# Kernel tuning notes

Measured on AMD Instinct MI355X. Metric: run time of the kernel, lower is better.

Reference implementation:

```python
import jax, jax.numpy as jnp
import numpy as np

N_EMBD = 1024
N_HEAD = 16
EPS = 1e-5

def layer_norm(x, g, b):
    mu = jnp.mean(x, axis=-1, keepdims=True)
    var = jnp.mean(jnp.square(x - mu), axis=-1, keepdims=True)
    return (x - mu) * jax.lax.rsqrt(var + EPS) * g + b

def setup_inputs() -> dict:
    key = jax.random.key(0)
    ks = jax.random.split(key, 12)
    C = N_EMBD
    s = lambda n: 1.0 / np.sqrt(n)
    return {
        "x": jax.random.normal(ks[0], (4, 2048, C), dtype=jnp.float32),
        "ln1_g": jnp.ones((C,), jnp.float32),
        "ln1_b": jnp.zeros((C,), jnp.float32),
        "attn_w": jax.random.normal(ks[1], (C, 3 * C), dtype=jnp.float32) * s(C),
        "attn_b": jnp.zeros((3 * C,), jnp.float32),
        "proj_w": jax.random.normal(ks[2], (C, C), dtype=jnp.float32) * s(C),
        "proj_b": jnp.zeros((C,), jnp.float32),
        "ln2_g": jnp.ones((C,), jnp.float32),
        "ln2_b": jnp.zeros((C,), jnp.float32),
        "fc1_w": jax.random.normal(ks[3], (C, 4 * C), dtype=jnp.float32) * s(C),
        "fc1_b": jnp.zeros((4 * C,), jnp.float32),
        "fc2_w": jax.random.normal(ks[4], (4 * C, C), dtype=jnp.float32) * s(4 * C),
        "fc2_b": jnp.zeros((C,), jnp.float32),
    }

def reference(x, ln1_g, ln1_b, attn_w, attn_b, proj_w, proj_b,
              ln2_g, ln2_b, fc1_w, fc1_b, fc2_w, fc2_b):
    B, T, C = x.shape
    H = N_HEAD
    D = C // H

    # --- self attention on ln1(x) ---
    h = layer_norm(x, ln1_g, ln1_b)
    qkv = h @ attn_w + attn_b                       # [B,T,3C]
    q, k, v = jnp.split(qkv, 3, axis=-1)
    q = q.reshape(B, T, H, D).transpose(0, 2, 1, 3)  # [B,H,T,D]
    k = k.reshape(B, T, H, D).transpose(0, 2, 1, 3)
    v = v.reshape(B, T, H, D).transpose(0, 2, 1, 3)
    att = jnp.einsum("bhqd,bhkd->bhqk", q, k) * (D ** -0.5)
    causal = jnp.tril(jnp.ones((T, T), dtype=bool))
    att = jnp.where(causal[None, None], att, -jnp.inf)
    att = jax.nn.softmax(att, axis=-1)
    y = jnp.einsum("bhqk,bhkd->bhqd", att, v)        # [B,H,T,D]
    y = y.transpose(0, 2, 1, 3).reshape(B, T, C)
    y = y @ proj_w + proj_b
    x = x + y

    # --- MLP on ln2(x) ---
    h = layer_norm(x, ln2_g, ln2_b)
    h = jax.nn.relu(h @ fc1_w + fc1_b)
    h = h @ fc2_w + fc2_b
    return x + h
```

## Files before the change

### kernel.cpp

```cpp
#include <hip/hip_runtime.h>
#include <cstdint>
#include <cstddef>

typedef __bf16 bf16x8 __attribute__((ext_vector_type(8)));
typedef float f32x4 __attribute__((ext_vector_type(4)));
typedef float f32x16 __attribute__((ext_vector_type(16)));
typedef unsigned short u16;
typedef unsigned uint2v __attribute__((ext_vector_type(2)));

namespace {
constexpr int Bb = 4, Tt = 2048, Cc = 1024, Hh = 16, Dd = 64;
constexpr int ROWS = Bb * Tt;
constexpr int C3 = 3 * Cc;
constexpr float LNEPS = 1e-5f;
constexpr float SCL2 = 0.18033688011112042f;
}

__device__ __forceinline__ u16 f2bf(float f) {
  union { float f; unsigned u; } v; v.f = f;
  return (u16)((v.u + 0x7fffu + ((v.u >> 16) & 1u)) >> 16);
}
__device__ __forceinline__ u16 bfn(float f) {
  union { __bf16 b; u16 u; } t; t.b = (__bf16)f; return t.u;
}
__device__ __forceinline__ unsigned pk2(float lo, float hi) {
  union { __bf16 b[2]; unsigned u; } t;
  t.b[0] = (__bf16)lo; t.b[1] = (__bf16)hi;
  return t.u;
}
__device__ __forceinline__ float exp2_hw(float x) {
  float r;
  asm("v_exp_f32 %0, %1" : "=v"(r) : "v"(x));
  return r;
}
__device__ __forceinline__ uint2v plswap(unsigned a, unsigned b) {
  return __builtin_amdgcn_permlane32_swap(a, b, false, false);
}
__device__ __forceinline__ float xhalf_max(float x) {
  union { float f; unsigned u; } c; c.f = x;
  uint2v r = plswap(c.u, c.u);
  union { unsigned u; float f; } a, b; a.u = r[0]; b.u = r[1];
  return fmaxf(a.f, b.f);
}
__device__ __forceinline__ float xhalf_sum(float x) {
  union { float f; unsigned u; } c; c.f = x;
  uint2v r = plswap(c.u, c.u);
  union { unsigned u; float f; } a, b; a.u = r[0]; b.u = r[1];
  return a.f + b.f;
}

typedef __attribute__((address_space(3))) unsigned lds_u32;
typedef __attribute__((address_space(1))) const unsigned glb_u32;
__device__ __forceinline__ void gload_lds16(const u16* g, u16* l) {
  __builtin_amdgcn_global_load_lds((glb_u32*)g, (lds_u32*)l, 16, 0, 0);
}

__global__ __launch_bounds__(256) void ln_kernel(
    const float* __restrict__ x, const float* __restrict__ g,
    const float* __restrict__ b, u16* __restrict__ out)
{
  const int row = blockIdx.x;
  const int tid = threadIdx.x;
  const float4 v = reinterpret_cast<const float4*>(x + (size_t)row * Cc)[tid];
  float s  = v.x + v.y + v.z + v.w;
  float ss = v.x * v.x + v.y * v.y + v.z * v.z + v.w * v.w;
#pragma unroll
  for (int off = 32; off; off >>= 1) {
    s  += __shfl_xor(s, off);
    ss += __shfl_xor(ss, off);
  }
  __shared__ float sa[4], sb[4];
  const int w = tid >> 6;
  if ((tid & 63) == 0) { sa[w] = s; sb[w] = ss; }
  __syncthreads();
  s  = sa[0] + sa[1] + sa[2] + sa[3];
  ss = sb[0] + sb[1] + sb[2] + sb[3];
  const float mu   = s * (1.0f / Cc);
  const float var  = ss * (1.0f / Cc) - mu * mu;
  const float rstd = rsqrtf(var + LNEPS);
  const float4 gv = reinterpret_cast<const float4*>(g)[tid];
  const float4 bv = reinterpret_cast<const float4*>(b)[tid];
  ushort4 o;
  o.x = f2bf((v.x - mu) * rstd * gv.x + bv.x);
  o.y = f2bf((v.y - mu) * rstd * gv.y + bv.y);
  o.z = f2bf((v.z - mu) * rstd * gv.z + bv.z);
  o.w = f2bf((v.w - mu) * rstd * gv.w + bv.w);
  reinterpret_cast<ushort4*>(out + (size_t)row * Cc)[tid] = o;
}

__global__ __launch_bounds__(256) void wcast_t(
    const float* __restrict__ w, u16* __restrict__ wt, int K, int N)
{
  __shared__ float tile[32][33];
  const int n0 = blockIdx.x * 32, k0 = blockIdx.y * 32;
  const int tx = threadIdx.x & 31, ty = threadIdx.x >> 5;
#pragma unroll
  for (int i = 0; i < 4; i++)
    tile[ty + i * 8][tx] = w[(size_t)(k0 + ty + i * 8) * N + n0 + tx];
  __syncthreads();
#pragma unroll
  for (int i = 0; i < 4; i++)
    wt[(size_t)(n0 + ty + i * 8) * K + k0 + tx] = f2bf(tile[tx][ty + i * 8]);
}

enum { EPI_BIAS_BF16 = 0, EPI_BIAS_RELU_BF16 = 1, EPI_BIAS_RES_F32 = 2 };

template <int EPI>
__global__ __launch_bounds__(512, 2) void gemm256(
    const u16* __restrict__ A, const u16* __restrict__ Bt,
    const float* __restrict__ bias, const float* __restrict__ res,
    void* __restrict__ outp, int M, int N, int K)
{
  __shared__ alignas(16) u16 Al[4][256 * 32];
  __shared__ alignas(16) u16 Bl[4][256 * 32];

  const int tid  = threadIdx.x;
  const int lane = tid & 63;
  const int wv   = tid >> 6;
  const int wr   = wv >> 2, wc = wv & 3;
  const int lr   = lane & 15;
  const int lg   = (lane >> 4) & 3;

  const int xcd = (int)blockIdx.x & 7;
  const int j   = (int)blockIdx.x >> 3;
  const int nbn = N >> 8;
  const int bmpx = ((int)gridDim.x >> 3) / nbn;
  const int bm = (xcd * bmpx + j / nbn) << 8;
  const int bn = (j % nbn) << 8;

  const int srl  = tid >> 2;
  const int schk = (tid & 3) ^ ((tid >> 3) & 3);
  const u16* gA = A  + (size_t)(bm + srl) * K + schk * 8;
  const u16* gB = Bt + (size_t)(bn + srl) * K + schk * 8;
  const size_t rowK128 = (size_t)128 * K;

  const int fsw  = (lg ^ ((lr >> 1) & 3)) * 8;
  const int arow = wr * 128 + lr;
  const int brow = wc * 64 + lr;

  f32x4 acc[8][4];
#pragma unroll
  for (int mi = 0; mi < 8; mi++)
#pragma unroll
    for (int nj = 0; nj < 4; nj++)
      acc[mi][nj] = (f32x4){0.f, 0.f, 0.f, 0.f};

  const int NT = K >> 5;

  auto stageA = [&](int t) {
    u16* d = &Al[t & 3][tid * 8];
    gload_lds16(gA + (size_t)t * 32, d);
    gload_lds16(gA + rowK128 + (size_t)t * 32, d + 4096);
  };
  auto stageB = [&](int t) {
    u16* d = &Bl[t & 3][tid * 8];
    gload_lds16(gB + (size_t)t * 32, d);
    gload_lds16(gB + rowK128 + (size_t)t * 32, d + 4096);
  };

  for (int t = 0; t < 3; ++t) { stageA(t); stageB(t); }
  asm volatile("s_waitcnt vmcnt(8)" ::: "memory");
  asm volatile("s_barrier" ::: "memory");

  for (int kt = 0; kt < NT; ++kt) {
    const u16* Ab = &Al[kt & 3][0];
    const u16* Bb = &Bl[kt & 3][0];
    const bool st = (kt + 3 < NT);

    bf16x8 bf[4];
#pragma unroll
    for (int nj = 0; nj < 4; ++nj)
      bf[nj] = *reinterpret_cast<const bf16x8*>(Bb + (brow + nj * 16) * 32 + fsw);
    bf16x8 af[4];
#pragma unroll
    for (int m = 0; m < 4; ++m)
      af[m] = *reinterpret_cast<const bf16x8*>(Ab + (arow + m * 16) * 32 + fsw);
    if (st) stageA(kt + 3);
    asm volatile("s_barrier" ::: "memory");
    __builtin_amdgcn_s_setprio(1);
#pragma unroll
    for (int m = 0; m < 4; ++m)
#pragma unroll
      for (int nj = 0; nj < 4; ++nj)
        acc[m][nj] = __builtin_amdgcn_mfma_f32_16x16x32_bf16(af[m], bf[nj], acc[m][nj], 0, 0, 0);
    __builtin_amdgcn_s_setprio(0);
    asm volatile("s_barrier" ::: "memory");

#pragma unroll
    for (int m = 0; m < 4; ++m)
      af[m] = *reinterpret_cast<const bf16x8*>(Ab + (arow + (m + 4) * 16) * 32 + fsw);
    if (st) stageB(kt + 3);
    if (kt < NT - 3)       { asm volatile("s_waitcnt vmcnt(8)" ::: "memory"); }
    else if (kt == NT - 3) { asm volatile("s_waitcnt vmcnt(4)" ::: "memory"); }
    else if (kt == NT - 2) { asm volatile("s_waitcnt vmcnt(0)" ::: "memory"); }
    asm volatile("s_barrier" ::: "memory");
    __builtin_amdgcn_s_setprio(1);
#pragma unroll
    for (int m = 0; m < 4; ++m)
#pragma unroll
      for (int nj = 0; nj < 4; ++nj)
        acc[m + 4][nj] = __builtin_amdgcn_mfma_f32_16x16x32_bf16(af[m], bf[nj], acc[m + 4][nj], 0, 0, 0);
    __builtin_amdgcn_s_setprio(0);
    asm volatile("s_barrier" ::: "memory");
  }

#pragma unroll
  for (int mi = 0; mi < 8; ++mi) {
    const int row0 = bm + wr * 128 + mi * 16 + lg * 4;
#pragma unroll
    for (int nj = 0; nj < 4; ++nj) {
      const int col = bn + wc * 64 + nj * 16 + lr;
      const float bv = bias[col];
#pragma unroll
      for (int r = 0; r < 4; ++r) {
        const int row = row0 + r;
        float v = acc[mi][nj][r] + bv;
        if constexpr (EPI == EPI_BIAS_RELU_BF16) v = fmaxf(v, 0.0f);
        if constexpr (EPI == EPI_BIAS_RES_F32) {
          float* out = (float*)outp;
          out[(size_t)row * N + col] = v + res[(size_t)row * N + col];
        } else {
          ((u16*)outp)[(size_t)row * N + col] = f2bf(v);
        }
      }
    }
  }
}

template <int EPI>
__global__ __launch_bounds__(256, 3) void gemm_bt2(
    const u16* __restrict__ A, const u16* __restrict__ Bt,
    const float* __restrict__ bias, const float* __restrict__ res,
    void* __restrict__ outp, int M, int N, int K)
{
  constexpr int BM = 128, BN = 128, BK = 64;
  __shared__ alignas(16) u16 As[BM][BK];
  __shared__ alignas(16) u16 Bs[BN][BK];
  const int tid  = threadIdx.x;
  const int lane = tid & 63;
  const int wv   = tid >> 6;
  const int wr   = wv >> 1, wc = wv & 1;
  const int lr   = lane & 15, lg = lane >> 4;

  const int xcd = (int)blockIdx.x & 7;
  const int j   = (int)blockIdx.x >> 3;
  const int bm = (xcd * 8 + (j >> 3)) << 7;
  const int bn = (j & 7) << 7;

  f32x4 acc[4][4];
#pragma unroll
  for (int mi = 0; mi < 4; mi++)
#pragma unroll
    for (int nj = 0; nj < 4; nj++)
      acc[mi][nj] = (f32x4){0.f, 0.f, 0.f, 0.f};

  const int srow = tid >> 3;
  const int scol = ((tid & 7) ^ (srow & 7)) * 8;
  const u16* ga = &A [(size_t)(bm + srow) * K + scol];
  const u16* gb = &Bt[(size_t)(bn + srow) * K + scol];
  u16* as_dst = &As[0][0] + (size_t)tid * 8;
  u16* bs_dst = &Bs[0][0] + (size_t)tid * 8;

  for (int k0 = 0; k0 < K; k0 += BK) {
#pragma unroll
    for (int p = 0; p < 4; p++) {
      gload_lds16(ga + (size_t)p * 32 * K + k0, as_dst + p * 2048);
      gload_lds16(gb + (size_t)p * 32 * K + k0, bs_dst + p * 2048);
    }
    __syncthreads();
#pragma unroll
    for (int kk = 0; kk < BK; kk += 32) {
      const int cb = kk >> 3;
      const int csw = ((cb + lg) ^ (lr & 7)) * 8;
      bf16x8 af[4], bfr[4];
#pragma unroll
      for (int mi = 0; mi < 4; mi++)
        af[mi] = *reinterpret_cast<const bf16x8*>(&As[wr * 64 + mi * 16 + lr][0] + csw);
#pragma unroll
      for (int nj = 0; nj < 4; nj++)
        bfr[nj] = *reinterpret_cast<const bf16x8*>(&Bs[wc * 64 + nj * 16 + lr][0] + csw);
#pragma unroll
      for (int mi = 0; mi < 4; mi++)
#pragma unroll
        for (int nj = 0; nj < 4; nj++)
          acc[mi][nj] = __builtin_amdgcn_mfma_f32_16x16x32_bf16(af[mi], bfr[nj], acc[mi][nj], 0, 0, 0);
    }
    __syncthreads();
  }

#pragma unroll
  for (int mi = 0; mi < 4; mi++) {
#pragma unroll
    for (int nj = 0; nj < 4; nj++) {
      const int col = bn + wc * 64 + nj * 16 + lr;
      const float bv = bias[col];
#pragma unroll
      for (int r = 0; r < 4; r++) {
        const int row = bm + wr * 64 + mi * 16 + lg * 4 + r;
        float v = acc[mi][nj][r] + bv;
        if constexpr (EPI == EPI_BIAS_RELU_BF16) v = fmaxf(v, 0.0f);
        if constexpr (EPI == EPI_BIAS_RES_F32) {
          float* out = (float*)outp;
          out[(size_t)row * N + col] = v + res[(size_t)row * N + col];
        } else {
          ((u16*)outp)[(size_t)row * N + col] = f2bf(v);
        }
      }
    }
  }
}

__global__ __launch_bounds__(256) void build_vt(
    const u16* __restrict__ qkv, u16* __restrict__ vt)
{
  __shared__ u16 tile[64][80];
  const int t0 = blockIdx.x * 64;
  const int h  = blockIdx.y;
  const int b  = blockIdx.z;
  const int tid = threadIdx.x;
  const int rr = tid >> 3, cc = (tid & 7) * 8;
#pragma unroll
  for (int p = 0; p < 2; p++) {
    const int t = rr + p * 32;
    bf16x8 v = *reinterpret_cast<const bf16x8*>(
        &qkv[(size_t)(b * Tt + t0 + t) * C3 + 2 * Cc + h * Dd + cc]);
    *reinterpret_cast<bf16x8*>(&tile[t][cc]) = v;
  }
  __syncthreads();
#pragma unroll
  for (int p = 0; p < 2; p++) {
    const int d = rr + p * 32;
    union { u16 u[8]; int4 v; } o;
#pragma unroll
    for (int j = 0; j < 8; j++) o.u[j] = tile[cc + j][d];
    *reinterpret_cast<int4*>(&vt[(size_t)((b * Hh + h) * Dd + d) * Tt + t0 + cc]) = o.v;
  }
}

__global__ __launch_bounds__(512, 2) void flash_attn(
    const u16* __restrict__ qkv,
    const u16* __restrict__ vt,
    u16* __restrict__ y)
{
  const int tid = threadIdx.x, lane = tid & 63, wv = tid >> 6;
  const int l31 = lane & 31, hf = lane >> 5;

  const int bid = blockIdx.x;
  const int lid = (bid & 7) * 32 + (bid >> 3);
  const int bh = lid >> 2, pg = lid & 3;
  const int b = bh >> 4, h = bh & 15;
  const int sbase = pg * 4 + (wv & 3);
  const int s = (wv < 4) ? sbase : (31 - sbase);

  const u16* qbase = qkv + (size_t)b * Tt * C3 + h * Dd;
  const u16* kbase = qbase + Cc;
  const u16* vbase = vt + (size_t)bh * Dd * Tt;

  bool dmask[16];
#pragma unroll
  for (int r = 0; r < 16; r++)
    dmask[r] = ((r & 3) + 8 * (r >> 2) + 4 * hf) > l31;

  const int qa0 = s * 64;
  const int qb0 = qa0 + 32;
  const int ta = 2 * s;

  bf16x8 qfa[4], qfb[4];
#pragma unroll
  for (int kc = 0; kc < 4; kc++) {
    qfa[kc] = *reinterpret_cast<const bf16x8*>(
        &qbase[(size_t)(qa0 + l31) * C3 + kc * 16 + hf * 8]);
    qfb[kc] = *reinterpret_cast<const bf16x8*>(
        &qbase[(size_t)(qb0 + l31) * C3 + kc * 16 + hf * 8]);
  }

  f32x16 oa[2], ob[2];
#pragma unroll
  for (int i = 0; i < 16; i++) { oa[0][i] = 0.f; oa[1][i] = 0.f; ob[0][i] = 0.f; ob[1][i] = 0.f; }
  float mA = -INFINITY, lA = 0.0f, mB = -INFINITY, lB = 0.0f;

  const u16* kptr = &kbase[(size_t)l31 * C3 + hf * 8];
  const u16* vp0 = &vbase[(size_t)l31 * Tt + hf * 8];
  const u16* vp1 = vp0 + (size_t)32 * Tt;

  bf16x8 kf[4];
#pragma unroll
  for (int kc = 0; kc < 4; kc++)
    kf[kc] = *reinterpret_cast<const bf16x8*>(kptr + kc * 16);

  for (int kt = 0; kt <= ta; ++kt) {
    bf16x8 vf[2][2];
#pragma unroll
    for (int ch = 0; ch < 2; ch++) {
      vf[0][ch] = *reinterpret_cast<const bf16x8*>(vp0 + ch * 16);
      vf[1][ch] = *reinterpret_cast<const bf16x8*>(vp1 + ch * 16);
    }
    vp0 += 32; vp1 += 32;

    f32x16 sA, sB;
#pragma unroll
    for (int i = 0; i < 16; i++) { sA[i] = 0.f; sB[i] = 0.f; }
#pragma unroll
    for (int kc = 0; kc < 4; kc++) {
      sA = __builtin_amdgcn_mfma_f32_32x32x16_bf16(kf[kc], qfa[kc], sA, 0, 0, 0);
      sB = __builtin_amdgcn_mfma_f32_32x32x16_bf16(kf[kc], qfb[kc], sB, 0, 0, 0);
    }

    kptr += (size_t)32 * C3;
    bf16x8 kn[4];
#pragma unroll
    for (int kc = 0; kc < 4; kc++)
      kn[kc] = *reinterpret_cast<const bf16x8*>(kptr + kc * 16);

    const bool diagA = (kt == ta);

    float svA[16], svB[16];
#pragma unroll
    for (int r = 0; r < 16; r++) {
      svA[r] = sA[r];
      if (diagA && dmask[r]) svA[r] = -INFINITY;
      svB[r] = sB[r];
    }

    float mAa = fmaxf(fmaxf(svA[0], svA[1]), fmaxf(svA[2], svA[3]));
    float mAb = fmaxf(fmaxf(svA[4], svA[5]), fmaxf(svA[6], svA[7]));
    float mAc = fmaxf(fmaxf(svA[8], svA[9]), fmaxf(svA[10], svA[11]));
    float mAd = fmaxf(fmaxf(svA[12], svA[13]), fmaxf(svA[14], svA[15]));
    float m8A = fmaxf(fmaxf(mAa, mAb), fmaxf(mAc, mAd));
    float mBa = fmaxf(fmaxf(svB[0], svB[1]), fmaxf(svB[2], svB[3]));
    float mBb = fmaxf(fmaxf(svB[4], svB[5]), fmaxf(svB[6], svB[7]));
    float mBc = fmaxf(fmaxf(svB[8], svB[9]), fmaxf(svB[10], svB[11]));
    float mBd = fmaxf(fmaxf(svB[12], svB[13]), fmaxf(svB[14], svB[15]));
    float m8B = fmaxf(fmaxf(mBa, mBb), fmaxf(mBc, mBd));
    m8A = xhalf_max(m8A);
    m8B = xhalf_max(m8B);

    if (!__all(m8A - mA <= 64.0f)) {
      const float mnew  = fmaxf(mA, m8A);
      const float alpha = exp2_hw((mA - mnew) * SCL2);
      lA *= alpha;
#pragma unroll
      for (int i = 0; i < 16; i++) { oa[0][i] *= alpha; oa[1][i] *= alpha; }
      mA = mnew;
    }
    if (!__all(m8B - mB <= 64.0f)) {
      const float mnew  = fmaxf(mB, m8B);
      const float alpha = exp2_hw((mB - mnew) * SCL2);
      lB *= alpha;
#pragma unroll
      for (int i = 0; i < 16; i++) { ob[0][i] *= alpha; ob[1][i] *= alpha; }
      mB = mnew;
    }

    const float msA = mA * SCL2;
    const float msB = mB * SCL2;
    float pA[16], pB[16];
#pragma unroll
    for (int r = 0; r < 16; r++) {
      pA[r] = exp2_hw(fmaf(svA[r], SCL2, -msA));
      pB[r] = exp2_hw(fmaf(svB[r], SCL2, -msB));
    }
    {
      float a0 = ((pA[0] + pA[1]) + (pA[2] + pA[3])) + ((pA[4] + pA[5]) + (pA[6] + pA[7]));
      float a1 = ((pA[8] + pA[9]) + (pA[10] + pA[11])) + ((pA[12] + pA[13]) + (pA[14] + pA[15]));
      lA += a0 + a1;
      float b0 = ((pB[0] + pB[1]) + (pB[2] + pB[3])) + ((pB[4] + pB[5]) + (pB[6] + pB[7]));
      float b1 = ((pB[8] + pB[9]) + (pB[10] + pB[11])) + ((pB[12] + pB[13]) + (pB[14] + pB[15]));
      lB += b0 + b1;
    }

    unsigned pwA[2][4], pwB[2][4];
#pragma unroll
    for (int ch = 0; ch < 2; ch++) {
      const int bs = ch * 8;
      {
        unsigned w0 = pk2(pA[bs + 0], pA[bs + 1]);
        unsigned w1 = pk2(pA[bs + 2], pA[bs + 3]);
        unsigned w2 = pk2(pA[bs + 4], pA[bs + 5]);
        unsigned w3 = pk2(pA[bs + 6], pA[bs + 7]);
        uint2v r02 = plswap(w0, w2);
        uint2v r13 = plswap(w1, w3);
        pwA[ch][0] = r02[0]; pwA[ch][2] = r02[1];
        pwA[ch][1] = r13[0]; pwA[ch][3] = r13[1];
      }
      {
        unsigned w0 = pk2(pB[bs + 0], pB[bs + 1]);
        unsigned w1 = pk2(pB[bs + 2], pB[bs + 3]);
        unsigned w2 = pk2(pB[bs + 4], pB[bs + 5]);
        unsigned w3 = pk2(pB[bs + 6], pB[bs + 7]);
        uint2v r02 = plswap(w0, w2);
        uint2v r13 = plswap(w1, w3);
        pwB[ch][0] = r02[0]; pwB[ch][2] = r02[1];
        pwB[ch][1] = r13[0]; pwB[ch][3] = r13[1];
      }
    }

#pragma unroll
    for (int d0i = 0; d0i < 2; d0i++)
#pragma unroll
      for (int ch = 0; ch < 2; ch++) {
        union { unsigned w[4]; bf16x8 v; } pa, pb;
        pa.w[0] = pwA[ch][0]; pa.w[1] = pwA[ch][1];
        pa.w[2] = pwA[ch][2]; pa.w[3] = pwA[ch][3];
        pb.w[0] = pwB[ch][0]; pb.w[1] = pwB[ch][1];
        pb.w[2] = pwB[ch][2]; pb.w[3] = pwB[ch][3];
        oa[d0i] = __builtin_amdgcn_mfma_f32_32x32x16_bf16(vf[d0i][ch], pa.v, oa[d0i], 0, 0, 0);
        ob[d0i] = __builtin_amdgcn_mfma_f32_32x32x16_bf16(vf[d0i][ch], pb.v, ob[d0i], 0, 0, 0);
      }

#pragma unroll
    for (int kc = 0; kc < 4; kc++) kf[kc] = kn[kc];
  }

  {
    bf16x8 vf[2][2];
#pragma unroll
    for (int ch = 0; ch < 2; ch++) {
      vf[0][ch] = *reinterpret_cast<const bf16x8*>(vp0 + ch * 16);
      vf[1][ch] = *reinterpret_cast<const bf16x8*>(vp1 + ch * 16);
    }

    f32x16 sB;
#pragma unroll
    for (int i = 0; i < 16; i++) sB[i] = 0.f;
#pragma unroll
    for (int kc = 0; kc < 4; kc++)
      sB = __builtin_amdgcn_mfma_f32_32x32x16_bf16(kf[kc], qfb[kc], sB, 0, 0, 0);

    float svB[16];
#pragma unroll
    for (int r = 0; r < 16; r++) {
      svB[r] = sB[r];
      if (dmask[r]) svB[r] = -INFINITY;
    }
    float mBa = fmaxf(fmaxf(svB[0], svB[1]), fmaxf(svB[2], svB[3]));
    float mBb = fmaxf(fmaxf(svB[4], svB[5]), fmaxf(svB[6], svB[7]));
    float mBc = fmaxf(fmaxf(svB[8], svB[9]), fmaxf(svB[10], svB[11]));
    float mBd = fmaxf(fmaxf(svB[12], svB[13]), fmaxf(svB[14], svB[15]));
    float m8B = fmaxf(fmaxf(mBa, mBb), fmaxf(mBc, mBd));
    m8B = xhalf_max(m8B);

    if (!__all(m8B - mB <= 64.0f)) {
      const float mnew  = fmaxf(mB, m8B);
      const float alpha = exp2_hw((mB - mnew) * SCL2);
      lB *= alpha;
#pragma unroll
      for (int i = 0; i < 16; i++) { ob[0][i] *= alpha; ob[1][i] *= alpha; }
      mB = mnew;
    }
    const float msB = mB * SCL2;
    float pB[16];
#pragma unroll
    for (int r = 0; r < 16; r++)
      pB[r] = exp2_hw(fmaf(svB[r], SCL2, -msB));
    {
      float b0 = ((pB[0] + pB[1]) + (pB[2] + pB[3])) + ((pB[4] + pB[5]) + (pB[6] + pB[7]));
      float b1 = ((pB[8] + pB[9]) + (pB[10] + pB[11])) + ((pB[12] + pB[13]) + (pB[14] + pB[15]));
      lB += b0 + b1;
    }
    unsigned pwB[2][4];
#pragma unroll
    for (int ch = 0; ch < 2; ch++) {
      const int bs = ch * 8;
      unsigned w0 = pk2(pB[bs + 0], pB[bs + 1]);
      unsigned w1 = pk2(pB[bs + 2], pB[bs + 3]);
      unsigned w2 = pk2(pB[bs + 4], pB[bs + 5]);
      unsigned w3 = pk2(pB[bs + 6], pB[bs + 7]);
      uint2v r02 = plswap(w0, w2);
      uint2v r13 = plswap(w1, w3);
      pwB[ch][0] = r02[0]; pwB[ch][2] = r02[1];
      pwB[ch][1] = r13[0]; pwB[ch][3] = r13[1];
    }
#pragma unroll
    for (int d0i = 0; d0i < 2; d0i++)
#pragma unroll
      for (int ch = 0; ch < 2; ch++) {
        union { unsigned w[4]; bf16x8 v; } pb;
        pb.w[0] = pwB[ch][0]; pb.w[1] = pwB[ch][1];
        pb.w[2] = pwB[ch][2]; pb.w[3] = pwB[ch][3];
        ob[d0i] = __builtin_amdgcn_mfma_f32_32x32x16_bf16(vf[d0i][ch], pb.v, ob[d0i], 0, 0, 0);
      }
  }

  {
    const float lsA = xhalf_sum(lA);
    const float invA = 1.0f / lsA;
    u16* yrow = y + (size_t)(b * Tt + qa0 + l31) * Cc + h * Dd;
#pragma unroll
    for (int d0i = 0; d0i < 2; d0i++)
#pragma unroll
      for (int qd = 0; qd < 4; qd++) {
        ushort4 o;
        o.x = bfn(oa[d0i][qd * 4 + 0] * invA);
        o.y = bfn(oa[d0i][qd * 4 + 1] * invA);
        o.z = bfn(oa[d0i][qd * 4 + 2] * invA);
        o.w = bfn(oa[d0i][qd * 4 + 3] * invA);
        *reinterpret_cast<ushort4*>(&yrow[d0i * 32 + qd * 8 + hf * 4]) = o;
      }
  }
  {
    const float lsB = xhalf_sum(lB);
    const float invB = 1.0f / lsB;
    u16* yrow = y + (size_t)(b * Tt + qb0 + l31) * Cc + h * Dd;
#pragma unroll
    for (int d0i = 0; d0i < 2; d0i++)
#pragma unroll
      for (int qd = 0; qd < 4; qd++) {
        ushort4 o;
        o.x = bfn(ob[d0i][qd * 4 + 0] * invB);
        o.y = bfn(ob[d0i][qd * 4 + 1] * invB);
        o.z = bfn(ob[d0i][qd * 4 + 2] * invB);
        o.w = bfn(ob[d0i][qd * 4 + 3] * invB);
        *reinterpret_cast<ushort4*>(&yrow[d0i * 32 + qd * 8 + hf * 4]) = o;
      }
  }
}

extern "C" void kernel_launch(void* const* d_in, const int* in_sizes, int n_in,
                              void* d_out, int out_size, void* d_ws, size_t ws_size,
                              hipStream_t stream)
{
  const float* x      = (const float*)d_in[0];
  const float* ln1_g  = (const float*)d_in[1];
  const float* ln1_b  = (const float*)d_in[2];
  const float* attn_w = (const float*)d_in[3];
  const float* attn_b = (const float*)d_in[4];
  const float* proj_w = (const float*)d_in[5];
  const float* proj_b = (const float*)d_in[6];
  const float* ln2_g  = (const float*)d_in[7];
  const float* ln2_b  = (const float*)d_in[8];
  const float* fc1_w  = (const float*)d_in[9];
  const float* fc1_b  = (const float*)d_in[10];
  const float* fc2_w  = (const float*)d_in[11];
  const float* fc2_b  = (const float*)d_in[12];
  float* out = (float*)d_out;

  char* ws = (char*)d_ws;
  size_t o = 0;
  auto alloc = [&](size_t bytes) { char* p = ws + o; o += bytes; return p; };
  u16* wqkv_t  = (u16*)alloc((size_t)C3 * Cc * 2);
  u16* wproj_t = (u16*)alloc((size_t)Cc * Cc * 2);
  u16* wfc1_t  = (u16*)alloc((size_t)4096 * Cc * 2);
  u16* wfc2_t  = (u16*)alloc((size_t)Cc * 4096 * 2);
  u16* h_bf    = (u16*)alloc((size_t)ROWS * Cc * 2);
  u16* y_bf    = (u16*)alloc((size_t)ROWS * Cc * 2);
  u16* qkv_raw = (u16*)alloc((size_t)ROWS * C3 * 2);
  u16* vt      = (u16*)alloc((size_t)Bb * Hh * Dd * Tt * 2);
  u16* hh      = qkv_raw;

  wcast_t<<<dim3(C3 / 32, Cc / 32), 256, 0, stream>>>(attn_w, wqkv_t, Cc, C3);
  wcast_t<<<dim3(Cc / 32, Cc / 32), 256, 0, stream>>>(proj_w, wproj_t, Cc, Cc);
  wcast_t<<<dim3(4096 / 32, Cc / 32), 256, 0, stream>>>(fc1_w, wfc1_t, Cc, 4096);
  wcast_t<<<dim3(Cc / 32, 4096 / 32), 256, 0, stream>>>(fc2_w, wfc2_t, 4096, Cc);

  ln_kernel<<<ROWS, 256, 0, stream>>>(x, ln1_g, ln1_b, h_bf);
  gemm256<EPI_BIAS_BF16><<<32 * (C3 / 256), 512, 0, stream>>>(
      h_bf, wqkv_t, attn_b, nullptr, qkv_raw, ROWS, C3, Cc);
  build_vt<<<dim3(Tt / 64, Hh, Bb), 256, 0, stream>>>(qkv_raw, vt);
  flash_attn<<<dim3(256), 512, 0, stream>>>(qkv_raw, vt, y_bf);
  gemm_bt2<EPI_BIAS_RES_F32><<<512, 256, 0, stream>>>(
      y_bf, wproj_t, proj_b, x, out, ROWS, Cc, Cc);
  ln_kernel<<<ROWS, 256, 0, stream>>>(out, ln2_g, ln2_b, h_bf);
  gemm256<EPI_BIAS_RELU_BF16><<<32 * (4096 / 256), 512, 0, stream>>>(
      h_bf, wfc1_t, fc1_b, nullptr, hh, ROWS, 4096, Cc);
  gemm_bt2<EPI_BIAS_RES_F32><<<512, 256, 0, stream>>>(
      hh, wfc2_t, fc2_b, out, out, ROWS, Cc, 4096);
}
```

Before: 365.2 us.

## Restructure 256x256 GEMM into 8-phase ping-pong pipeline with BK=64 half-tiles

Replaces the 4-stage BK=32 GEMM used for the QKV and FC1 projections with a double-buffered BK=64 kernel. Each 256x256 tile is split into A and B halves of 128 rows, and the work runs as four MFMA phases. The next tile's half loads are interleaved between phases using explicit vmcnt waits and barriers. Warp-to-output mapping changes so each warp covers scattered 64x32 sub-blocks, which means more LDS reads and barriers per tile in exchange for larger K chunks. The gemm_bt2 grid mapping is generalized to compute the tile count from N, which leaves the launch configuration the same.

Result: no change. 359.6 us (-1.5%).

```diff
diff --git a/kernel.cpp b/kernel.cpp
--- a/kernel.cpp
+++ b/kernel.cpp
@@ -106,20 +106,21 @@
 enum { EPI_BIAS_BF16 = 0, EPI_BIAS_RELU_BF16 = 1, EPI_BIAS_RES_F32 = 2 };
 
 template <int EPI>
-__global__ __launch_bounds__(512, 2) void gemm256(
+__global__ __launch_bounds__(512, 2) void gemm8p(
     const u16* __restrict__ A, const u16* __restrict__ Bt,
     const float* __restrict__ bias, const float* __restrict__ res,
     void* __restrict__ outp, int M, int N, int K)
 {
-  __shared__ alignas(16) u16 Al[4][256 * 32];
-  __shared__ alignas(16) u16 Bl[4][256 * 32];
-
-  const int tid  = threadIdx.x;
-  const int lane = tid & 63;
-  const int wv   = tid >> 6;
-  const int wr   = wv >> 2, wc = wv & 3;
-  const int lr   = lane & 15;
-  const int lg   = (lane >> 4) & 3;
+  __shared__ alignas(16) u16 Asl[2][2][128 * 64];
+  __shared__ alignas(16) u16 Bsl[2][2][128 * 64];
+
+  const int tid = threadIdx.x;
+  const int l   = tid & 63;
+  const int wv  = tid >> 6;
+  const int wr  = wv >> 2;
+  const int wc  = wv & 3;
+  const int lr  = l & 15;
+  const int lg  = (l >> 4) & 3;
 
   const int xcd = (int)blockIdx.x & 7;
   const int j   = (int)blockIdx.x >> 3;
@@ -128,15 +129,14 @@
   const int bm = (xcd * bmpx + j / nbn) << 8;
   const int bn = (j % nbn) << 8;
 
-  const int srl  = tid >> 2;
-  const int schk = (tid & 3) ^ ((tid >> 3) & 3);
-  const u16* gA = A  + (size_t)(bm + srl) * K + schk * 8;
-  const u16* gB = Bt + (size_t)(bn + srl) * K + schk * 8;
-  const size_t rowK128 = (size_t)128 * K;
-
-  const int fsw  = (lg ^ ((lr >> 1) & 3)) * 8;
-  const int arow = wr * 128 + lr;
-  const int brow = wc * 64 + lr;
+  const int srw = wv * 8 + (l >> 3);
+  const int sch = ((l & 7) ^ ((l >> 3) & 7)) * 8;
+  const int dst = (l & 7) * 8;
+
+  const int csw0 = (lg ^ (lr & 7)) * 8;
+  const int csw1 = ((4 + lg) ^ (lr & 7)) * 8;
+  const int ar = wr * 64;
+  const int br = wc * 32;
 
   f32x4 acc[8][4];
 #pragma unroll
@@ -145,71 +145,117 @@
     for (int nj = 0; nj < 4; nj++)
       acc[mi][nj] = (f32x4){0.f, 0.f, 0.f, 0.f};
 
-  const int NT = K >> 5;
-
-  auto stageA = [&](int t) {
-    u16* d = &Al[t & 3][tid * 8];
-    gload_lds16(gA + (size_t)t * 32, d);
-    gload_lds16(gA + rowK128 + (size_t)t * 32, d + 4096);
+  const int NT = K >> 6;
+
+  auto stA = [&](int h, int tt) {
+#pragma unroll
+    for (int L = 0; L < 2; ++L)
+      gload_lds16(A + (size_t)(bm + h * 128 + L * 64 + srw) * K + tt * 64 + sch,
+                  &Asl[tt & 1][h][(L * 64 + srw) * 64 + dst]);
   };
-  auto stageB = [&](int t) {
-    u16* d = &Bl[t & 3][tid * 8];
-    gload_lds16(gB + (size_t)t * 32, d);
-    gload_lds16(gB + rowK128 + (size_t)t * 32, d + 4096);
+  auto stB = [&](int h, int tt) {
+#pragma unroll
+    for (int L = 0; L < 2; ++L)
+      gload_lds16(Bt + (size_t)(bn + h * 128 + L * 64 + srw) * K + tt * 64 + sch,
+                  &Bsl[tt & 1][h][(L * 64 + srw) * 64 + dst]);
   };
 
-  for (int t = 0; t < 3; ++t) { stageA(t); stageB(t); }
-  asm volatile("s_waitcnt vmcnt(8)" ::: "memory");
+  stA(0, 0); stB(0, 0); stB(1, 0); stA(1, 0);
+  asm volatile("s_waitcnt vmcnt(4)" ::: "memory");
   asm volatile("s_barrier" ::: "memory");
 
-  for (int kt = 0; kt < NT; ++kt) {
-    const u16* Ab = &Al[kt & 3][0];
-    const u16* Bb = &Bl[kt & 3][0];
-    const bool st = (kt + 3 < NT);
-
-    bf16x8 bf[4];
-#pragma unroll
-    for (int nj = 0; nj < 4; ++nj)
-      bf[nj] = *reinterpret_cast<const bf16x8*>(Bb + (brow + nj * 16) * 32 + fsw);
-    bf16x8 af[4];
-#pragma unroll
-    for (int m = 0; m < 4; ++m)
-      af[m] = *reinterpret_cast<const bf16x8*>(Ab + (arow + m * 16) * 32 + fsw);
-    if (st) stageA(kt + 3);
+  bf16x8 af[4][2], bfr[2][2][2];
+
+  for (int t = 0; t < NT; ++t) {
+    const int cb = t & 1;
+    const bool st = (t + 1 < NT);
+    const u16* Ah0 = &Asl[cb][0][0];
+    const u16* Ah1 = &Asl[cb][1][0];
+    const u16* Bh0 = &Bsl[cb][0][0];
+    const u16* Bh1 = &Bsl[cb][1][0];
+
+#pragma unroll
+    for (int m = 0; m < 4; ++m) {
+      af[m][0] = *reinterpret_cast<const bf16x8*>(Ah0 + (ar + m * 16 + lr) * 64 + csw0);
+      af[m][1] = *reinterpret_cast<const bf16x8*>(Ah0 + (ar + m * 16 + lr) * 64 + csw1);
+    }
+#pragma unroll
+    for (int n = 0; n < 2; ++n) {
+      bfr[0][n][0] = *reinterpret_cast<const bf16x8*>(Bh0 + (br + n * 16 + lr) * 64 + csw0);
+      bfr[0][n][1] = *reinterpret_cast<const bf16x8*>(Bh0 + (br + n * 16 + lr) * 64 + csw1);
+    }
+    if (st) { stA(0, t + 1); stB(0, t + 1); }
     asm volatile("s_barrier" ::: "memory");
     __builtin_amdgcn_s_setprio(1);
 #pragma unroll
     for (int m = 0; m < 4; ++m)
 #pragma unroll
-      for (int nj = 0; nj < 4; ++nj)
-        acc[m][nj] = __builtin_amdgcn_mfma_f32_16x16x32_bf16(af[m], bf[nj], acc[m][nj], 0, 0, 0);
+      for (int n = 0; n < 2; ++n) {
+        acc[m][n] = __builtin_amdgcn_mfma_f32_16x16x32_bf16(af[m][0], bfr[0][n][0], acc[m][n], 0, 0, 0);
+        acc[m][n] = __builtin_amdgcn_mfma_f32_16x16x32_bf16(af[m][1], bfr[0][n][1], acc[m][n], 0, 0, 0);
+      }
+    __builtin_amdgcn_s_setprio(0);
+    if (st) asm volatile("s_waitcnt vmcnt(6)" ::: "memory");
+    else    asm volatile("s_waitcnt vmcnt(2)" ::: "memory");
+    asm volatile("s_barrier" ::: "memory");
+
+#pragma unroll
+    for (int n = 0; n < 2; ++n) {
+      bfr[1][n][0] = *reinterpret_cast<const bf16x8*>(Bh1 + (br + n * 16 + lr) * 64 + csw0);
+      bfr[1][n][1] = *reinterpret_cast<const bf16x8*>(Bh1 + (br + n * 16 + lr) * 64 + csw1);
+    }
+    if (st) stB(1, t + 1);
+    asm volatile("s_barrier" ::: "memory");
+    __builtin_amdgcn_s_setprio(1);
+#pragma unroll
+    for (int m = 0; m < 4; ++m)
+#pragma unroll
+      for (int n = 0; n < 2; ++n) {
+        acc[m][2 + n] = __builtin_amdgcn_mfma_f32_16x16x32_bf16(af[m][0], bfr[1][n][0], acc[m][2 + n], 0, 0, 0);
+        acc[m][2 + n] = __builtin_amdgcn_mfma_f32_16x16x32_bf16(af[m][1], bfr[1][n][1], acc[m][2 + n], 0, 0, 0);
+      }
+    __builtin_amdgcn_s_setprio(0);
+    if (st) asm volatile("s_waitcnt vmcnt(6)" ::: "memory");
+    else    asm volatile("s_waitcnt vmcnt(0)" ::: "memory");
+    asm volatile("s_barrier" ::: "memory");
+
+#pragma unroll
+    for (int m = 0; m < 4; ++m) {
+      af[m][0] = *reinterpret_cast<const bf16x8*>(Ah1 + (ar + m * 16 + lr) * 64 + csw0);
+      af[m][1] = *reinterpret_cast<const bf16x8*>(Ah1 + (ar + m * 16 + lr) * 64 + csw1);
+    }
+    if (st) stA(1, t + 1);
+    asm volatile("s_barrier" ::: "memory");
+    __builtin_amdgcn_s_setprio(1);
+#pragma unroll
+    for (int m = 0; m < 4; ++m)
+#pragma unroll
+      for (int n = 0; n < 2; ++n) {
+        acc[4 + m][n] = __builtin_amdgcn_mfma_f32_16x16x32_bf16(af[m][0], bfr[0][n][0], acc[4 + m][n], 0, 0, 0);
+        acc[4 + m][n] = __builtin_amdgcn_mfma_f32_16x16x32_bf16(af[m][1], bfr[0][n][1], acc[4 + m][n], 0, 0, 0);
+      }
     __builtin_amdgcn_s_setprio(0);
     asm volatile("s_barrier" ::: "memory");
 
+    __builtin_amdgcn_s_setprio(1);
 #pragma unroll
     for (int m = 0; m < 4; ++m)
-      af[m] = *reinterpret_cast<const bf16x8*>(Ab + (arow + (m + 4) * 16) * 32 + fsw);
-    if (st) stageB(kt + 3);
-    if (kt < NT - 3)       { asm volatile("s_waitcnt vmcnt(8)" ::: "memory"); }
-    else if (kt == NT - 3) { asm volatile("s_waitcnt vmcnt(4)" ::: "memory"); }
-    else if (kt == NT - 2) { asm volatile("s_waitcnt vmcnt(0)" ::: "memory"); }
+#pragma unroll
+      for (int n = 0; n < 2; ++n) {
+        acc[4 + m][2 + n] = __builtin_amdgcn_mfma_f32_16x16x32_bf16(af[m][0], bfr[1][n][0], acc[4 + m][2 + n], 0, 0, 0);
+        acc[4 + m][2 + n] = __builtin_amdgcn_mfma_f32_16x16x32_bf16(af[m][1], bfr[1][n][1], acc[4 + m][2 + n], 0, 0, 0);
+      }
+    __builtin_amdgcn_s_setprio(0);
+    if (st) asm volatile("s_waitcnt vmcnt(4)" ::: "memory");
     asm volatile("s_barrier" ::: "memory");
-    __builtin_amdgcn_s_setprio(1);
-#pragma unroll
-    for (int m = 0; m < 4; ++m)
-#pragma unroll
-      for (int nj = 0; nj < 4; ++nj)
-        acc[m + 4][nj] = __builtin_amdgcn_mfma_f32_16x16x32_bf16(af[m], bf[nj], acc[m + 4][nj], 0, 0, 0);
-    __builtin_amdgcn_s_setprio(0);
-    asm volatile("s_barrier" ::: "memory");
   }
 
 #pragma unroll
   for (int mi = 0; mi < 8; ++mi) {
-    const int row0 = bm + wr * 128 + mi * 16 + lg * 4;
+    const int row0 = bm + (mi >> 2) * 128 + wr * 64 + (mi & 3) * 16 + lg * 4;
 #pragma unroll
     for (int nj = 0; nj < 4; ++nj) {
-      const int col = bn + wc * 64 + nj * 16 + lr;
+      const int col = bn + (nj >> 1) * 128 + wc * 32 + (nj & 1) * 16 + lr;
       const float bv = bias[col];
 #pragma unroll
       for (int r = 0; r < 4; ++r) {
@@ -244,8 +290,10 @@
 
   const int xcd = (int)blockIdx.x & 7;
   const int j   = (int)blockIdx.x >> 3;
-  const int bm = (xcd * 8 + (j >> 3)) << 7;
-  const int bn = (j & 7) << 7;
+  const int nbn = N >> 7;
+  const int bmpx = ((int)gridDim.x >> 3) / nbn;
+  const int bm = (xcd * bmpx + j / nbn) << 7;
+  const int bn = (j % nbn) << 7;
 
   f32x4 acc[4][4];
 #pragma unroll
@@ -654,15 +702,15 @@
   wcast_t<<<dim3(Cc / 32, 4096 / 32), 256, 0, stream>>>(fc2_w, wfc2_t, 4096, Cc);
 
   ln_kernel<<<ROWS, 256, 0, stream>>>(x, ln1_g, ln1_b, h_bf);
-  gemm256<EPI_BIAS_BF16><<<32 * (C3 / 256), 512, 0, stream>>>(
+  gemm8p<EPI_BIAS_BF16><<<8 * (ROWS / 256 / 8) * (C3 / 256), 512, 0, stream>>>(
       h_bf, wqkv_t, attn_b, nullptr, qkv_raw, ROWS, C3, Cc);
   build_vt<<<dim3(Tt / 64, Hh, Bb), 256, 0, stream>>>(qkv_raw, vt);
   flash_attn<<<dim3(256), 512, 0, stream>>>(qkv_raw, vt, y_bf);
-  gemm_bt2<EPI_BIAS_RES_F32><<<512, 256, 0, stream>>>(
+  gemm_bt2<EPI_BIAS_RES_F32><<<64 * (Cc / 128), 256, 0, stream>>>(
       y_bf, wproj_t, proj_b, x, out, ROWS, Cc, Cc);
   ln_kernel<<<ROWS, 256, 0, stream>>>(out, ln2_g, ln2_b, h_bf);
-  gemm256<EPI_BIAS_RELU_BF16><<<32 * (4096 / 256), 512, 0, stream>>>(
+  gemm8p<EPI_BIAS_RELU_BF16><<<8 * (ROWS / 256 / 8) * (4096 / 256), 512, 0, stream>>>(
       h_bf, wfc1_t, fc1_b, nullptr, hh, ROWS, 4096, Cc);
-  gemm_bt2<EPI_BIAS_RES_F32><<<512, 256, 0, stream>>>(
+  gemm_bt2<EPI_BIAS_RES_F32><<<64 * (Cc / 128), 256, 0, stream>>>(
       hh, wfc2_t, fc2_b, out, out, ROWS, Cc, 4096);
 }
```
